# Optimization experiments

Measured on AMD Instinct MI355X. Metric: run time of the kernel, lower is better.

Reference implementation:

```python
import jax, jax.numpy as jnp
import numpy as np

B, T = 256, 1024
V = 96      # vocab (input_size == output_size)
H = 128     # hidden_size


def setup_inputs() -> dict:
    key = jax.random.key(0)
    ks = jax.random.split(key, 12)
    s = 0.05
    return {
        "x": jax.random.randint(ks[0], (B, T), 0, V),
        "emb": jax.random.normal(ks[1], (V, H), jnp.float32) * s,
        "W_ih0": jax.random.normal(ks[2], (H, H), jnp.float32) * s,
        "W_hh0": jax.random.normal(ks[3], (H, H), jnp.float32) * s,
        "b_ih0": jax.random.normal(ks[4], (H,), jnp.float32) * s,
        "b_hh0": jax.random.normal(ks[5], (H,), jnp.float32) * s,
        "W_ih1": jax.random.normal(ks[6], (H, H), jnp.float32) * s,
        "W_hh1": jax.random.normal(ks[7], (H, H), jnp.float32) * s,
        "b_ih1": jax.random.normal(ks[8], (H,), jnp.float32) * s,
        "b_hh1": jax.random.normal(ks[9], (H,), jnp.float32) * s,
        "fc_W": jax.random.normal(ks[10], (V, H), jnp.float32) * s,
        "fc_b": jax.random.normal(ks[11], (V,), jnp.float32) * s,
    }


def _rnn_layer(xs, W_ih, W_hh, b_ih, b_hh):
    # xs: [B, T, H]. PyTorch RNN: h_t = tanh(W_ih x_t + b_ih + W_hh h_{t-1} + b_hh)
    xp = jnp.einsum("bth,oh->bto", xs, W_ih) + (b_ih + b_hh)  # hoist input proj out of scan

    def step(h, xt):  # h: [B,H], xt: [B,H]
        h = jnp.tanh(xt + h @ W_hh.T)
        return h, h

    h0 = jnp.zeros((xs.shape[0], W_hh.shape[0]), xs.dtype)
    hT, ys = jax.lax.scan(step, h0, xp.transpose(1, 0, 2))  # scan over time
    return ys.transpose(1, 0, 2), hT


def reference(x, emb, W_ih0, W_hh0, b_ih0, b_hh0, W_ih1, W_hh1, b_ih1, b_hh1, fc_W, fc_b):
    xe = emb[x]                                   # [B, T, H] embedding lookup
    y0, h0 = _rnn_layer(xe, W_ih0, W_hh0, b_ih0, b_hh0)
    y1, h1 = _rnn_layer(y0, W_ih1, W_hh1, b_ih1, b_hh1)
    out = y1.reshape(-1, H) @ fc_W.T + fc_b        # [B*T, V]
    hidden = jnp.stack([h0, h1], axis=0)           # [num_layers, B, H]
    return out, hidden
```

## Files before the change

### kernel.cpp

```cpp
#include <hip/hip_runtime.h>
#include <hip/hip_bf16.h>


#define B_SZ 256
#define T_LEN 1024
#define HD 128
#define VC 96
#define OUT_MAIN (B_SZ * T_LEN * VC)
#define HID_OFF OUT_MAIN

#define NB 16
#define NBLK (B_SZ / NB)
#define NT 512
#define EPH 132
#define HCH 136

typedef _Float16 h8v __attribute__((ext_vector_type(8)));
typedef _Float16 h4v __attribute__((ext_vector_type(4)));
typedef _Float16 h2v __attribute__((ext_vector_type(2)));
typedef float f4v __attribute__((ext_vector_type(4)));

#define MM(A, Bf, C) __builtin_amdgcn_mfma_f32_16x16x32_f16(A, Bf, C, 0, 0, 0)

#define BARRIER()                                          \
  do {                                                     \
    asm volatile("s_waitcnt lgkmcnt(0)" ::: "memory");     \
    __builtin_amdgcn_s_barrier();                          \
    asm volatile("" ::: "memory");                         \
  } while (0)

__device__ __forceinline__ float bf2f(__hip_bfloat16 v) { return __bfloat162float(v); }

__device__ __forceinline__ bool detect_f32(const void* emb) {
  const unsigned short* u = (const unsigned short*)emb;
  int hits = 0;
#pragma unroll
  for (int i = 0; i < 128; ++i) hits += (((u[i] >> 7) & 0xFF) >= 127);
  return hits > 2;
}

__device__ __forceinline__ float ldw(const void* p, int i, bool f32) {
  return f32 ? ((const float*)p)[i] : bf2f(((const __hip_bfloat16*)p)[i]);
}

__device__ __forceinline__ float tanh_fast(float x) {
  const float e = exp2f(x * 2.885390082f);
  const float r = __builtin_amdgcn_rcpf(e + 1.0f);
  return fmaf(-2.0f, r, 1.0f);
}

__device__ __forceinline__ unsigned short f2bfbits(float x) {
  unsigned u = __float_as_uint(x);
  unsigned r = (u + 0x7fffu + ((u >> 16) & 1u)) >> 16;
  return (unsigned short)r;
}

__device__ __forceinline__ unsigned cvt_pk_bf16(float lo, float hi) {
  unsigned r;
  asm("v_cvt_pk_bf16_f32 %0, %1, %2" : "=v"(r) : "v"(lo), "v"(hi));
  return r;
}

__global__ __launch_bounds__(128) void embp_kernel(
    const void* __restrict__ emb, const void* __restrict__ Wih0,
    const void* __restrict__ bih0, const void* __restrict__ bhh0,
    float* __restrict__ embp) {
  const bool f32 = detect_f32(emb);
  __shared__ float ev[HD];
  const int v = blockIdx.x, r = threadIdx.x;
  ev[r] = ldw(emb, v * HD + r, f32);
  __syncthreads();
  float acc = ldw(bih0, r, f32) + ldw(bhh0, r, f32);
#pragma unroll 8
  for (int j = 0; j < HD; ++j) acc += ldw(Wih0, r * HD + j, f32) * ev[j];
  embp[v * HD + r] = acc;
}

template <bool USE_WS>
__global__ __launch_bounds__(NT, 2) void rnn_mfma(
    const int* __restrict__ x,
    const float* __restrict__ embp_g,
    const void* __restrict__ emb,
    const void* __restrict__ Wih0,
    const void* __restrict__ bih0,
    const void* __restrict__ bhh0,
    const void* __restrict__ Whh0,
    const void* __restrict__ Wih1,
    const void* __restrict__ Whh1,
    const void* __restrict__ bih1,
    const void* __restrict__ bhh1,
    const void* __restrict__ fcW,
    const void* __restrict__ fcb_g,
    void* __restrict__ out) {
  __shared__ __align__(16) _Float16 embp16[VC * EPH];
  __shared__ __align__(16) _Float16 hb0[2][16 * HCH];
  __shared__ __align__(16) _Float16 hb1[2][16 * HCH];
  __shared__ __align__(16) unsigned char xb8[(T_LEN + 2) * NB];

  const int tid = threadIdx.x;
  const int lane = tid & 63;
  const int w = tid >> 6;
  const int lm = lane & 15;
  const int lg = lane >> 4;
  const bool f32 = detect_f32(emb);
  const int bbase = blockIdx.x * NB;

  for (int i = tid; i < NB * T_LEN; i += NT) {
    const int m = i >> 10, t = i & (T_LEN - 1);
    xb8[t * 16 + m] = (unsigned char)x[(bbase + m) * T_LEN + t];
  }
  if (tid < 2 * NB) {
    const int t = T_LEN + (tid >> 4), m = tid & 15;
    xb8[t * 16 + m] = (unsigned char)x[(bbase + m) * T_LEN + (T_LEN - 1)];
  }

  if constexpr (USE_WS) {
    const float2* src = (const float2*)embp_g;
    for (int i = tid; i < VC * 64; i += NT) {
      const int v = i >> 6, j = i & 63;
      const float2 f = src[i];
      h2v p; p[0] = (_Float16)f.x; p[1] = (_Float16)f.y;
      ((h2v*)embp16)[v * (EPH / 2) + j] = p;
    }
  } else {
    const int r = tid & 127, vg = tid >> 7;
    const float bsum = ldw(bih0, r, f32) + ldw(bhh0, r, f32);
    for (int vi = 0; vi < 24; ++vi) {
      const int v = vg * 24 + vi;
      float acc = bsum;
#pragma unroll 8
      for (int k = 0; k < HD; ++k)
        acc += ldw(Wih0, r * HD + k, f32) * ldw(emb, v * HD + k, f32);
      embp16[v * EPH + r] = (_Float16)acc;
    }
  }

  for (int i = tid; i < 16 * HCH; i += NT) {
    ((unsigned*)hb0)[i] = 0u;
    ((unsigned*)hb1)[i] = 0u;
  }

  const bool fcact = (w < 6);

  h8v w0[4], wi[4], wh[4], wf[4];
  {
    const int n = 16 * w + lm;
#pragma unroll
    for (int kt = 0; kt < 4; ++kt)
#pragma unroll
      for (int j = 0; j < 8; ++j) {
        const int k = kt * 32 + lg * 8 + j;
        w0[kt][j] = (_Float16)ldw(Whh0, n * HD + k, f32);
        wi[kt][j] = (_Float16)ldw(Wih1, n * HD + k, f32);
        wh[kt][j] = (_Float16)ldw(Whh1, n * HD + k, f32);
        wf[kt][j] = (_Float16)(fcact ? ldw(fcW, n * HD + k, f32) : 0.0f);
      }
  }
  f4v b1v, fcv;
#pragma unroll
  for (int r = 0; r < 4; ++r) {
    const int c = 16 * w + 4 * lg + r;
    b1v[r] = ldw(bih1, c, f32) + ldw(bhh1, c, f32);
    fcv[r] = fcact ? ldw(fcb_g, c, f32) : 0.0f;
  }

  const int rdb = lg * HCH + lm * 8;
  const int wofs = (2 * w + (lg >> 1)) * HCH + lm * 8 + 4 * (lg & 1);
  const int gofs = 16 * w + 4 * lg;

  __syncthreads();

  h4v epc;
  int xcur;
  const unsigned char* xbp = &xb8[2 * 16 + lm];
  {
    const int x0 = xb8[0 * 16 + lm];
    xcur = xb8[1 * 16 + lm];
    epc = *(const h4v*)&embp16[x0 * EPH + gofs];
  }

  char* po = (char*)out;
  long ostride = 0;
  if (fcact) {
    const long e0 = (long)(bbase + lm) * T_LEN * VC + 16 * w + 4 * lg;
    po = (char*)out + e0 * (f32 ? 4 : 2);
    ostride = (long)VC * (f32 ? 4 : 2);
  }

#define STEP(Q, P, DO_H0, DO_H1, DO_OUT)                                       \
  do {                                                                         \
    h8v h0f[4], h1f[4];                                                        \
    if (DO_H0 || DO_H1) {                                                      \
      _Pragma("unroll") for (int kt = 0; kt < 4; ++kt)                         \
          h0f[kt] = *(const h8v*)&hb0[Q][rdb + kt * 4 * HCH];                  \
    }                                                                          \
    _Pragma("unroll") for (int kt = 0; kt < 4; ++kt)                           \
        h1f[kt] = *(const h8v*)&hb1[Q][rdb + kt * 4 * HCH];                    \
    int xnext_ = 0;                                                            \
    h4v epn_ = epc;                                                            \
    if (DO_H0) {                                                               \
      xnext_ = *xbp; xbp += 16;                                                \
      epn_ = *(const h4v*)&embp16[xcur * EPH + gofs];                          \
    }                                                                          \
    if (DO_H0) {                                                               \
      f4v a0 = {(float)epc[0], (float)epc[1], (float)epc[2], (float)epc[3]};   \
      a0 = MM(w0[0], h0f[0], a0); a0 = MM(w0[1], h0f[1], a0);                  \
      a0 = MM(w0[2], h0f[2], a0); a0 = MM(w0[3], h0f[3], a0);                  \
      h4v o;                                                                   \
      _Pragma("unroll") for (int r = 0; r < 4; ++r)                            \
          o[r] = (_Float16)tanh_fast(a0[r]);                                   \
      *(h4v*)&hb0[P][wofs] = o;                                                \
    }                                                                          \
    if (DO_H1) {                                                               \
      f4v a1 = MM(wi[0], h0f[0], b1v);                                         \
      a1 = MM(wi[1], h0f[1], a1); a1 = MM(wi[2], h0f[2], a1);                  \
      a1 = MM(wi[3], h0f[3], a1);                                              \
      a1 = MM(wh[0], h1f[0], a1); a1 = MM(wh[1], h1f[1], a1);                  \
      a1 = MM(wh[2], h1f[2], a1); a1 = MM(wh[3], h1f[3], a1);                  \
      h4v o;                                                                   \
      _Pragma("unroll") for (int r = 0; r < 4; ++r)                            \
          o[r] = (_Float16)tanh_fast(a1[r]);                                   \
      *(h4v*)&hb1[P][wofs] = o;                                                \
    }                                                                          \
    if (DO_OUT && fcact) {                                                     \
      f4v a2 = MM(wf[0], h1f[0], fcv);                                         \
      a2 = MM(wf[1], h1f[1], a2); a2 = MM(wf[2], h1f[2], a2);                  \
      a2 = MM(wf[3], h1f[3], a2);                                              \
      if (f32) {                                                               \
        *(f4v*)po = a2;                                                        \
      } else {                                                                 \
        uint2 u;                                                               \
        u.x = cvt_pk_bf16(a2[0], a2[1]);                                       \
        u.y = cvt_pk_bf16(a2[2], a2[3]);                                       \
        *(uint2*)po = u;                                                       \
      }                                                                        \
      po += ostride;                                                           \
    }                                                                          \
    BARRIER();                                                                 \
    if (DO_H0) { epc = epn_; xcur = xnext_; }                                  \
  } while (0)

  STEP(1, 0, true, false, false);
  STEP(0, 1, true, true, false);
#pragma unroll 1
  for (int tt = 2; tt < T_LEN; tt += 2) {
    STEP(1, 0, true, true, true);
    STEP(0, 1, true, true, true);
  }
  STEP(1, 0, false, true, true);
  STEP(0, 1, false, false, true);
#undef STEP

  float* outf = (float*)out;
  unsigned short* outu = (unsigned short*)out;

  if (tid < 256) {
    const int m = tid >> 4, ch = tid & 15;
    const h8v v0 = *(const h8v*)&hb0[(T_LEN - 1) & 1][ch * HCH + m * 8];
    const h8v v1 = *(const h8v*)&hb1[T_LEN & 1][ch * HCH + m * 8];
    const long i0 = HID_OFF + (long)(bbase + m) * HD + ch * 8;
    const long i1 = i0 + (long)B_SZ * HD;
    if (f32) {
#pragma unroll
      for (int j = 0; j < 8; ++j) {
        outf[i0 + j] = (float)v0[j];
        outf[i1 + j] = (float)v1[j];
      }
    } else {
#pragma unroll
      for (int j = 0; j < 8; ++j) {
        outu[i0 + j] = f2bfbits((float)v0[j]);
        outu[i1 + j] = f2bfbits((float)v1[j]);
      }
    }
  }
}

extern "C" void kernel_launch(void* const* d_in, const int* in_sizes, int n_in,
                              void* d_out, int out_size, void* d_ws, size_t ws_size,
                              hipStream_t stream) {
  const int* x = (const int*)d_in[0];
  const void* emb = d_in[1];
  const void* Wih0 = d_in[2];
  const void* Whh0 = d_in[3];
  const void* bih0 = d_in[4];
  const void* bhh0 = d_in[5];
  const void* Wih1 = d_in[6];
  const void* Whh1 = d_in[7];
  const void* bih1 = d_in[8];
  const void* bhh1 = d_in[9];
  const void* fcW = d_in[10];
  const void* fcb = d_in[11];

  const size_t need = (size_t)VC * HD * sizeof(float);
  if (d_ws != nullptr && ws_size >= need) {
    float* embp = (float*)d_ws;
    embp_kernel<<<VC, HD, 0, stream>>>(emb, Wih0, bih0, bhh0, embp);
    rnn_mfma<true><<<NBLK, NT, 0, stream>>>(x, embp, emb, Wih0, bih0, bhh0,
                                            Whh0, Wih1, Whh1, bih1, bhh1,
                                            fcW, fcb, d_out);
  } else {
    rnn_mfma<false><<<NBLK, NT, 0, stream>>>(x, nullptr, emb, Wih0, bih0, bhh0,
                                             Whh0, Wih1, Whh1, bih1, bhh1,
                                             fcW, fcb, d_out);
  }
}
```

Measured before the change: 898.0 us.

## Interleave MFMA chains across layers and specialize dtype path at compile time

```diff
diff --git a/kernel.cpp b/kernel.cpp
--- a/kernel.cpp
+++ b/kernel.cpp
@@ -12,13 +12,15 @@
 #define NB 16
 #define NBLK (B_SZ / NB)
 #define NT 512
-#define EPH 132
+#define EPH 130
 #define HCH 136
 
 typedef _Float16 h8v __attribute__((ext_vector_type(8)));
 typedef _Float16 h4v __attribute__((ext_vector_type(4)));
 typedef _Float16 h2v __attribute__((ext_vector_type(2)));
 typedef float f4v __attribute__((ext_vector_type(4)));
+
+template <bool V> struct BoolT { static constexpr bool value = V; };
 
 #define MM(A, Bf, C) __builtin_amdgcn_mfma_f32_16x16x32_f16(A, Bf, C, 0, 0, 0)
 
@@ -170,63 +172,74 @@
 
   __syncthreads();
 
-  h4v epc;
-  int xcur;
-  const unsigned char* xbp = &xb8[2 * 16 + lm];
-  {
-    const int x0 = xb8[0 * 16 + lm];
-    xcur = xb8[1 * 16 + lm];
-    epc = *(const h4v*)&embp16[x0 * EPH + gofs];
-  }
-
-  char* po = (char*)out;
-  long ostride = 0;
-  if (fcact) {
-    const long e0 = (long)(bbase + lm) * T_LEN * VC + 16 * w + 4 * lg;
-    po = (char*)out + e0 * (f32 ? 4 : 2);
-    ostride = (long)VC * (f32 ? 4 : 2);
-  }
+  union EpU { uint2 u; h4v h; };
+
+  auto core = [&](auto f32tag) {
+    constexpr bool F32 = decltype(f32tag)::value;
+
+    h4v epc;
+    int xcur;
+    const unsigned char* xbp = &xb8[2 * 16 + lm];
+    {
+      const int x0 = xb8[0 * 16 + lm];
+      xcur = xb8[1 * 16 + lm];
+      const int gb = x0 * EPH + gofs;
+      EpU e;
+      e.u.x = *(const unsigned*)&embp16[gb];
+      e.u.y = *(const unsigned*)&embp16[gb + 2];
+      epc = e.h;
+    }
+
+    constexpr long OSTRIDE = (long)VC * (F32 ? 4 : 2);
+    char* po = (char*)out +
+               ((long)(bbase + lm) * T_LEN * VC + 16 * w + 4 * lg) * (F32 ? 4 : 2);
 
 #define STEP(Q, P, DO_H0, DO_H1, DO_OUT)                                       \
   do {                                                                         \
     h8v h0f[4], h1f[4];                                                        \
-    if (DO_H0 || DO_H1) {                                                      \
-      _Pragma("unroll") for (int kt = 0; kt < 4; ++kt)                         \
-          h0f[kt] = *(const h8v*)&hb0[Q][rdb + kt * 4 * HCH];                  \
-    }                                                                          \
-    _Pragma("unroll") for (int kt = 0; kt < 4; ++kt)                           \
-        h1f[kt] = *(const h8v*)&hb1[Q][rdb + kt * 4 * HCH];                    \
+    _Pragma("unroll") for (int kt = 0; kt < 4; ++kt) {                         \
+      if (DO_H0 || DO_H1) h0f[kt] = *(const h8v*)&hb0[Q][rdb + kt * 4 * HCH];  \
+      h1f[kt] = *(const h8v*)&hb1[Q][rdb + kt * 4 * HCH];                      \
+    }                                                                          \
     int xnext_ = 0;                                                            \
     h4v epn_ = epc;                                                            \
     if (DO_H0) {                                                               \
       xnext_ = *xbp; xbp += 16;                                                \
-      epn_ = *(const h4v*)&embp16[xcur * EPH + gofs];                          \
-    }                                                                          \
+      const int gb_ = xcur * EPH + gofs;                                       \
+      EpU e_;                                                                  \
+      e_.u.x = *(const unsigned*)&embp16[gb_];                                 \
+      e_.u.y = *(const unsigned*)&embp16[gb_ + 2];                             \
+      epn_ = e_.h;                                                             \
+    }                                                                          \
+    f4v a0, a1, a1c, a2;                                                       \
     if (DO_H0) {                                                               \
-      f4v a0 = {(float)epc[0], (float)epc[1], (float)epc[2], (float)epc[3]};   \
-      a0 = MM(w0[0], h0f[0], a0); a0 = MM(w0[1], h0f[1], a0);                  \
-      a0 = MM(w0[2], h0f[2], a0); a0 = MM(w0[3], h0f[3], a0);                  \
+      a0[0] = (float)epc[0]; a0[1] = (float)epc[1];                            \
+      a0[2] = (float)epc[2]; a0[3] = (float)epc[3];                            \
+    }                                                                          \
+    if (DO_H1) { a1 = b1v; a1c[0] = 0.f; a1c[1] = 0.f; a1c[2] = 0.f;           \
+                 a1c[3] = 0.f; }                                               \
+    if (DO_OUT) a2 = fcv;                                                      \
+    _Pragma("unroll") for (int kt = 0; kt < 4; ++kt) {                         \
+      if (DO_H0) a0 = MM(w0[kt], h0f[kt], a0);                                 \
+      if (DO_H1) a1 = MM(wi[kt], h0f[kt], a1);                                 \
+      if (DO_H1) a1c = MM(wh[kt], h1f[kt], a1c);                               \
+      if (DO_OUT) a2 = MM(wf[kt], h1f[kt], a2);                                \
+    }                                                                          \
+    if (DO_H0) {                                                               \
       h4v o;                                                                   \
       _Pragma("unroll") for (int r = 0; r < 4; ++r)                            \
           o[r] = (_Float16)tanh_fast(a0[r]);                                   \
       *(h4v*)&hb0[P][wofs] = o;                                                \
     }                                                                          \
     if (DO_H1) {                                                               \
-      f4v a1 = MM(wi[0], h0f[0], b1v);                                         \
-      a1 = MM(wi[1], h0f[1], a1); a1 = MM(wi[2], h0f[2], a1);                  \
-      a1 = MM(wi[3], h0f[3], a1);                                              \
-      a1 = MM(wh[0], h1f[0], a1); a1 = MM(wh[1], h1f[1], a1);                  \
-      a1 = MM(wh[2], h1f[2], a1); a1 = MM(wh[3], h1f[3], a1);                  \
+      const f4v s1 = a1 + a1c;                                                 \
       h4v o;                                                                   \
       _Pragma("unroll") for (int r = 0; r < 4; ++r)                            \
-          o[r] = (_Float16)tanh_fast(a1[r]);                                   \
+          o[r] = (_Float16)tanh_fast(s1[r]);                                   \
       *(h4v*)&hb1[P][wofs] = o;                                                \
     }                                                                          \
     if (DO_OUT && fcact) {                                                     \
-      f4v a2 = MM(wf[0], h1f[0], fcv);                                         \
-      a2 = MM(wf[1], h1f[1], a2); a2 = MM(wf[2], h1f[2], a2);                  \
-      a2 = MM(wf[3], h1f[3], a2);                                              \
-      if (f32) {                                                               \
+      if constexpr (F32) {                                                     \
         *(f4v*)po = a2;                                                        \
       } else {                                                                 \
         uint2 u;                                                               \
@@ -234,46 +247,50 @@
         u.y = cvt_pk_bf16(a2[2], a2[3]);                                       \
         *(uint2*)po = u;                                                       \
       }                                                                        \
-      po += ostride;                                                           \
+      po += OSTRIDE;                                                           \
     }                                                                          \
     BARRIER();                                                                 \
     if (DO_H0) { epc = epn_; xcur = xnext_; }                                  \
   } while (0)
 
-  STEP(1, 0, true, false, false);
-  STEP(0, 1, true, true, false);
+    STEP(1, 0, true, false, false);
+    STEP(0, 1, true, true, false);
 #pragma unroll 1
-  for (int tt = 2; tt < T_LEN; tt += 2) {
-    STEP(1, 0, true, true, true);
-    STEP(0, 1, true, true, true);
-  }
-  STEP(1, 0, false, true, true);
-  STEP(0, 1, false, false, true);
+    for (int tt = 2; tt < T_LEN; tt += 2) {
+      STEP(1, 0, true, true, true);
+      STEP(0, 1, true, true, true);
+    }
+    STEP(1, 0, false, true, true);
+    STEP(0, 1, false, false, true);
 #undef STEP
 
-  float* outf = (float*)out;
-  unsigned short* outu = (unsigned short*)out;
-
-  if (tid < 256) {
-    const int m = tid >> 4, ch = tid & 15;
-    const h8v v0 = *(const h8v*)&hb0[(T_LEN - 1) & 1][ch * HCH + m * 8];
-    const h8v v1 = *(const h8v*)&hb1[T_LEN & 1][ch * HCH + m * 8];
-    const long i0 = HID_OFF + (long)(bbase + m) * HD + ch * 8;
-    const long i1 = i0 + (long)B_SZ * HD;
-    if (f32) {
-#pragma unroll
-      for (int j = 0; j < 8; ++j) {
-        outf[i0 + j] = (float)v0[j];
-        outf[i1 + j] = (float)v1[j];
+    float* outf = (float*)out;
+    unsigned short* outu = (unsigned short*)out;
+
+    if (tid < 256) {
+      const int m = tid >> 4, ch = tid & 15;
+      const h8v v0 = *(const h8v*)&hb0[(T_LEN - 1) & 1][ch * HCH + m * 8];
+      const h8v v1 = *(const h8v*)&hb1[T_LEN & 1][ch * HCH + m * 8];
+      const long i0 = HID_OFF + (long)(bbase + m) * HD + ch * 8;
+      const long i1 = i0 + (long)B_SZ * HD;
+      if constexpr (F32) {
+#pragma unroll
+        for (int j = 0; j < 8; ++j) {
+          outf[i0 + j] = (float)v0[j];
+          outf[i1 + j] = (float)v1[j];
+        }
+      } else {
+#pragma unroll
+        for (int j = 0; j < 8; ++j) {
+          outu[i0 + j] = f2bfbits((float)v0[j]);
+          outu[i1 + j] = f2bfbits((float)v1[j]);
+        }
       }
-    } else {
-#pragma unroll
-      for (int j = 0; j < 8; ++j) {
-        outu[i0 + j] = f2bfbits((float)v0[j]);
-        outu[i1 + j] = f2bfbits((float)v1[j]);
-      }
-    }
-  }
+    }
+  };
+
+  if (f32) core(BoolT<true>{});
+  else core(BoolT<false>{});
 }
 
 extern "C" void kernel_launch(void* const* d_in, const int* in_sizes, int n_in,
```

Result: no change. 900.0 us (+0.2%).
